# Performance work log

Measured on AMD Instinct MI355X. Metric: run time of the kernel, lower is better.

The kernel has to match this reference:

```python
import jax, jax.numpy as jnp
import numpy as np

WINDOW = 7
EPS = 1e-8


def setup_inputs() -> dict:
    key = jax.random.key(0)
    k1, k2, k3 = jax.random.split(key, 3)
    x = jax.random.normal(k1, (8, 256, 64, 64), dtype=jnp.float32)
    # 1x1 conv weights (bias=False): [out_ch, in_ch]
    w_reduce = jax.random.normal(k2, (64, 256), dtype=jnp.float32) * 0.05
    w_proj = jax.random.normal(k3, (512, 64), dtype=jnp.float32) * 0.1
    return {"x": x, "w_reduce": w_reduce, "w_proj": w_proj}


def _unfold_window(feat, window):
    # feat: [b, c, h, w] -> patches: [b, c, window*window, h, w]
    b, c, h, w = feat.shape
    pad = window // 2
    fp = jnp.pad(feat, ((0, 0), (0, 0), (pad, pad), (pad, pad)))
    # fixed small loop over window^2 = 49 shifts (matches F.unfold ordering)
    return jnp.stack(
        [fp[:, :, i:i + h, j:j + w] for i in range(window) for j in range(window)],
        axis=2,
    )


def reference(x, w_reduce, w_proj):
    window = WINDOW
    # reduce: 1x1 conv, no bias
    feat = jnp.einsum('oc,bchw->bohw', w_reduce, x)  # [b, cr, h, w]
    patches = _unfold_window(feat, window)           # [b, cr, K, h, w], K=49
    # cosine similarity between center feature and each window patch (dim=channel)
    dot = jnp.einsum('bchw,bckhw->bkhw', feat, patches)          # [b, K, h, w]
    cn = jnp.sqrt(jnp.sum(feat * feat, axis=1))                  # [b, h, w]
    pn = jnp.sqrt(jnp.sum(patches * patches, axis=1))            # [b, K, h, w]
    sim = dot / jnp.maximum(cn[:, None] * pn, EPS)               # [b, K, h, w]
    att = jax.nn.softmax(sim, axis=1)                            # softmax over window dim
    corr = jnp.einsum('bkhw,bckhw->bchw', att, patches)          # [b, cr, h, w]
    # proj: 1x1 conv, no bias
    return jnp.einsum('oc,bchw->bohw', w_proj, corr)             # [b, out, h, w]
```

## Files before the change

### kernel.cpp

```cpp
#include <hip/hip_runtime.h>
#include <stdint.h>

#define NPIX 4096
#define CIN  256
#define CR   64
#define COUT 512
#define NB   8
#define CG   256
#define FT   128

typedef _Float16 half8 __attribute__((ext_vector_type(8)));
typedef _Float16 half4 __attribute__((ext_vector_type(4)));
typedef _Float16 half2v __attribute__((ext_vector_type(2)));
typedef float f32x4 __attribute__((ext_vector_type(4)));

__device__ __forceinline__ float dpp8_sum(float d) {
  int y;
  y = __builtin_amdgcn_update_dpp(0, __float_as_int(d), 0xB1, 0xF, 0xF, true);
  d += __int_as_float(y);
  y = __builtin_amdgcn_update_dpp(0, __float_as_int(d), 0x4E, 0xF, 0xF, true);
  d += __int_as_float(y);
  y = __builtin_amdgcn_update_dpp(0, __float_as_int(d), 0x141, 0xF, 0xF, true);
  d += __int_as_float(y);
  return d;
}

__global__ __launch_bounds__(256) void k0_prep(
    const float* __restrict__ wr, const float* __restrict__ wp,
    _Float16* __restrict__ wrAh, _Float16* __restrict__ wrAl,
    _Float16* __restrict__ wpH,
    float* __restrict__ icnG, float* __restrict__ featTail)
{
  const int tid = blockIdx.x * 256 + threadIdx.x;
  if (tid < 16384) {
    const int j = tid & 7, l = (tid >> 3) & 63;
    const int kt = (tid >> 9) & 7, mt = tid >> 12;
    const int m = mt * 16 + (l & 15);
    const int k = kt * 32 + (l >> 4) * 8 + j;
    const float v = wr[m * CIN + k];
    const _Float16 h = (_Float16)v;
    wrAh[tid] = h;
    wrAl[tid] = (_Float16)(v - (float)h);
  } else if (tid < 16384 + COUT * CR) {
    const int fi = tid - 16384;
    const int j = fi & 7, l = (fi >> 3) & 63;
    const int kt = (fi >> 9) & 1, ot = (fi >> 10) & 3, g = fi >> 12;
    const int o = g * 64 + ot * 16 + (l & 15);
    const int k = kt * 32 + (l >> 4) * 8 + j;
    wpH[fi] = (_Float16)wp[o * CR + k];
  } else {
    const int gi = tid - (16384 + COUT * CR);
    if (gi < CG)               icnG[gi] = 0.f;
    else if (gi < 2 * CG)      icnG[CG + NB * NPIX + (gi - CG)] = 0.f;
    else if (gi < 2 * CG + FT) featTail[gi - 2 * CG] = 0.f;
  }
}

__global__ __launch_bounds__(512) void k1_reduce(
    const float* __restrict__ x,
    const _Float16* __restrict__ wrAh, const _Float16* __restrict__ wrAl,
    _Float16* __restrict__ feat_h, float* __restrict__ icn)
{
  const int blk = blockIdx.x;
  const int b = blk >> 6, seg = blk & 63;
  const int t = threadIdx.x, lane = t & 63;
  const int g = __builtin_amdgcn_readfirstlane((int)t >> 6);
  const int nt = g & 3, mth = g >> 2;
  const int col = lane & 15, krow = lane >> 4;

  const float* xb = x + (size_t)b * CIN * NPIX + seg * 64 + nt * 16 + col;

  f32x4 c0 = {0.f, 0.f, 0.f, 0.f};
  f32x4 c1 = {0.f, 0.f, 0.f, 0.f};

#pragma unroll
  for (int kt = 0; kt < 8; ++kt) {
    half8 Bh, Bl;
    const float* xk = xb + (size_t)(kt * 32 + krow * 8) * NPIX;
#pragma unroll
    for (int j = 0; j < 8; ++j) {
      const float v = xk[(size_t)j * NPIX];
      const _Float16 h = (_Float16)v;
      Bh[j] = h;
      Bl[j] = (_Float16)(v - (float)h);
    }
    const int fi0 = ((mth * 2 + 0) * 8 + kt) * 512 + lane * 8;
    const int fi1 = ((mth * 2 + 1) * 8 + kt) * 512 + lane * 8;
    const half8 Ah0 = *(const half8*)(wrAh + fi0);
    const half8 Al0 = *(const half8*)(wrAl + fi0);
    const half8 Ah1 = *(const half8*)(wrAh + fi1);
    const half8 Al1 = *(const half8*)(wrAl + fi1);
    c0 = __builtin_amdgcn_mfma_f32_16x16x32_f16(Ah0, Bh, c0, 0, 0, 0);
    c0 = __builtin_amdgcn_mfma_f32_16x16x32_f16(Ah0, Bl, c0, 0, 0, 0);
    c0 = __builtin_amdgcn_mfma_f32_16x16x32_f16(Al0, Bh, c0, 0, 0, 0);
    c1 = __builtin_amdgcn_mfma_f32_16x16x32_f16(Ah1, Bh, c1, 0, 0, 0);
    c1 = __builtin_amdgcn_mfma_f32_16x16x32_f16(Ah1, Bl, c1, 0, 0, 0);
    c1 = __builtin_amdgcn_mfma_f32_16x16x32_f16(Al1, Bh, c1, 0, 0, 0);
  }

  const int px = seg * 64 + nt * 16 + col;
  _Float16* fb = feat_h + ((size_t)b * NPIX + px) * 64;
  const int ch0 = mth * 32 + krow * 4;
  half4 v0, v1;
  float p = 0.f;
#pragma unroll
  for (int r = 0; r < 4; ++r) {
    v0[r] = (_Float16)c0[r];
    v1[r] = (_Float16)c1[r];
    p = fmaf(c0[r], c0[r], p);
    p = fmaf(c1[r], c1[r], p);
  }
  *(half4*)(fb + ch0) = v0;
  *(half4*)(fb + ch0 + 16) = v1;

  p += __shfl_xor(p, 16);
  p += __shfl_xor(p, 32);

  __shared__ float cn[8][16];
  if (lane < 16) cn[g][lane] = p;
  __syncthreads();
  if (t < 64) {
    const int nt2 = t >> 4, c16 = t & 15;
    const float ss = cn[nt2][c16] + cn[nt2 + 4][c16];
    icn[b * NPIX + seg * 64 + t] = rsqrtf(fmaxf(ss, 1e-16f));
  }
}

__global__ __launch_bounds__(256, 4) void k23_fused(
    const _Float16* __restrict__ feat_h, const float* __restrict__ icn,
    const _Float16* __restrict__ wpH, float* __restrict__ out)
{
  const int blk = blockIdx.x;
  const int b = blk & 7;
  const int rest = blk >> 3;
  const int h = rest >> 1, s = rest & 1;
  const int t = threadIdx.x;
  const int lane = t & 63;
  const int wv = __builtin_amdgcn_readfirstlane((int)t >> 6);
  const int w = t >> 3;
  const int cb = (t & 7) * 8;
  const int wg = s * 32 + w;
  const int px = h * 64 + wg;
  const int gpx = b * NPIX + px;

  const float* cnb = icn + b * NPIX;

  __shared__ __align__(16) _Float16 fs[2][40][72];
  __shared__ float cnS[2][48];
  __shared__ __align__(16) _Float16 corrH[2048];

  half8 rS0, rS1;
  float ricn = 0.f;

  auto LOAD = [&](int ar) {
    const long base = ((long)b * NPIX + ar * 64 + s * 32 - 4) * 64;
    rS0 = *(const half8*)(feat_h + base + (long)t * 8);
    if (t < 64) rS1 = *(const half8*)(feat_h + base + (long)(256 + t) * 8);
    if (t < 40) ricn = cnb[ar * 64 + s * 32 - 4 + t];
  };
  auto WRITE = [&](int bufi) {
    *(half8*)&fs[bufi][t >> 3][(t & 7) * 8] = rS0;
    if (t < 64) *(half8*)&fs[bufi][32 + (t >> 3)][(t & 7) * 8] = rS1;
    if (t < 40) cnS[bufi][t] = ricn;
  };

  half2v fc2[4];
  {
    const half8 fcv = *(const half8*)(feat_h + ((size_t)b * NPIX + px) * 64 + cb);
#pragma unroll
    for (int i = 0; i < 4; ++i) { fc2[i][0] = fcv[2*i]; fc2[i][1] = fcv[2*i+1]; }
  }
  const float icnc = icn[gpx];

  half2v accA[4], accB[4];
#pragma unroll
  for (int i = 0; i < 4; ++i) {
    accA[i] = (half2v)(_Float16)0.f;
    accB[i] = (half2v)(_Float16)0.f;
  }

  const int lo = (h - 3 < 0) ? 0 : h - 3;
  const int hi = (h + 3 > 63) ? 63 : h + 3;
  float l = 7.0f * (float)(6 - (hi - lo));

  LOAD(lo);
  WRITE(0);
  __syncthreads();

  int buf = 0;
  for (int ar = lo; ar <= hi; ++ar) {
    if (ar < hi) LOAD(ar + 1);
#pragma unroll
    for (int dx = -3; dx <= 3; ++dx) {
      const int j = w + 4 + dx;
      const half8 nv = *(const half8*)&fs[buf][j][cb];
      half2v n0, n1, n2, n3;
      n0[0] = nv[0]; n0[1] = nv[1];
      n1[0] = nv[2]; n1[1] = nv[3];
      n2[0] = nv[4]; n2[1] = nv[5];
      n3[0] = nv[6]; n3[1] = nv[7];
      float d = 0.f;
      d = __builtin_amdgcn_fdot2(fc2[0], n0, d, false);
      d = __builtin_amdgcn_fdot2(fc2[1], n1, d, false);
      d = __builtin_amdgcn_fdot2(fc2[2], n2, d, false);
      d = __builtin_amdgcn_fdot2(fc2[3], n3, d, false);
      d = dpp8_sum(d);
      const float icnk = cnS[buf][j];
      float sim = d * icnc * icnk;
      const bool valid = (unsigned)(wg + dx) < 64u;
      sim = valid ? sim : 0.f;
      const float p = __expf(sim);
      l += p;
      const float pv = valid ? p : 0.f;
      const _Float16 ph = (_Float16)pv;
      half2v ph2; ph2[0] = ph; ph2[1] = ph;
      if (dx & 1) {
        accA[0] = ph2 * n0 + accA[0];
        accA[1] = ph2 * n1 + accA[1];
        accA[2] = ph2 * n2 + accA[2];
        accA[3] = ph2 * n3 + accA[3];
      } else {
        accB[0] = ph2 * n0 + accB[0];
        accB[1] = ph2 * n1 + accB[1];
        accB[2] = ph2 * n2 + accB[2];
        accB[3] = ph2 * n3 + accB[3];
      }
    }
    if (ar < hi) WRITE(buf ^ 1);
    __syncthreads();
    buf ^= 1;
  }

  {
    const float inv = __builtin_amdgcn_rcpf(l);
    half8 hv;
#pragma unroll
    for (int i = 0; i < 4; ++i) {
      const float a0 = (float)accA[i][0] + (float)accB[i][0];
      const float a1 = (float)accA[i][1] + (float)accB[i][1];
      hv[2*i]   = (_Float16)(a0 * inv);
      hv[2*i+1] = (_Float16)(a1 * inv);
    }
    const int wbyte = (w * 128 + (cb << 1)) ^ ((w & 7) << 4);
    *(half8*)((char*)corrH + wbyte) = hv;
  }
  __syncthreads();

  const char* cH = (const char*)corrH;
#pragma unroll
  for (int pt = 0; pt < 2; ++pt) {
    half8 Bf0, Bf1;
    {
      const int pxl = pt * 16 + (lane & 15);
      const int sw = (pxl & 7) << 4;
      const int rowb = pxl * 128 + ((lane >> 4) << 4);
      Bf0 = *(const half8*)(cH + (rowb ^ sw));
      Bf1 = *(const half8*)(cH + ((rowb + 64) ^ sw));
    }
#pragma unroll
    for (int ot = 0; ot < 8; ++ot) {
      const int T = wv * 8 + ot;
      f32x4 c = {0.f, 0.f, 0.f, 0.f};
      const half8 A0 = *(const half8*)(wpH + (size_t)(T * 2 + 0) * 512 + lane * 8);
      const half8 A1 = *(const half8*)(wpH + (size_t)(T * 2 + 1) * 512 + lane * 8);
      c = __builtin_amdgcn_mfma_f32_16x16x32_f16(A0, Bf0, c, 0, 0, 0);
      c = __builtin_amdgcn_mfma_f32_16x16x32_f16(A1, Bf1, c, 0, 0, 0);
      float* op = out + ((size_t)b * COUT + T * 16 + ((lane >> 4) << 2)) * NPIX
                      + h * 64 + s * 32 + pt * 16 + (lane & 15);
#pragma unroll
      for (int r = 0; r < 4; ++r) op[(size_t)r * NPIX] = c[r];
    }
  }
}

extern "C" void kernel_launch(void* const* d_in, const int* in_sizes, int n_in,
                              void* d_out, int out_size, void* d_ws, size_t ws_size,
                              hipStream_t stream)
{
  const float* x  = (const float*)d_in[0];
  const float* wr = (const float*)d_in[1];
  const float* wp = (const float*)d_in[2];
  float* out = (float*)d_out;

  float* ws = (float*)d_ws;
  _Float16* wrAh  = (_Float16*)ws;
  _Float16* wrAl  = (_Float16*)(ws + 8192);
  _Float16* wpH   = (_Float16*)(ws + 16384);
  float* icnG     = ws + 32768;
  float* icn      = icnG + CG;
  _Float16* feat_h = (_Float16*)(icn + NB * NPIX + CG);
  float* featTail = (float*)(feat_h + (size_t)NB * NPIX * 64);

  hipLaunchKernelGGL(k0_prep,   dim3(195),  dim3(256), 0, stream, wr, wp, wrAh, wrAl, wpH, icnG, featTail);
  hipLaunchKernelGGL(k1_reduce, dim3(512),  dim3(512), 0, stream, x, wrAh, wrAl, feat_h, icn);
  hipLaunchKernelGGL(k23_fused, dim3(1024), dim3(256), 0, stream, feat_h, icn, wpH, out);
}
```

Before: 39.79 us.

## Prefetch two rows ahead and reuse weight fragments across pixel tiles

The row-staging pipeline now keeps two rows of global loads in flight in registers (distance-2 prefetch), so global latency is hidden over a longer compute span. The projection loop is restructured so each weight fragment pair is loaded once and applied to both 16-pixel tiles, halving global weight loads, with s_setprio raised around the MFMA block. Stores from both tiles are interleaved. This costs extra registers for the second prefetch buffer, which could reduce occupancy.

```diff
diff --git a/kernel.cpp b/kernel.cpp
--- a/kernel.cpp
+++ b/kernel.cpp
@@ -149,19 +149,25 @@
   __shared__ float cnS[2][48];
   __shared__ __align__(16) _Float16 corrH[2048];
 
-  half8 rS0, rS1;
-  float ricn = 0.f;
-
-  auto LOAD = [&](int ar) {
+  half8 pS0, pS1, nS0, nS1;
+  float pIc = 0.f, nIc = 0.f;
+
+  auto LOADP = [&](int ar) {
     const long base = ((long)b * NPIX + ar * 64 + s * 32 - 4) * 64;
-    rS0 = *(const half8*)(feat_h + base + (long)t * 8);
-    if (t < 64) rS1 = *(const half8*)(feat_h + base + (long)(256 + t) * 8);
-    if (t < 40) ricn = cnb[ar * 64 + s * 32 - 4 + t];
+    pS0 = *(const half8*)(feat_h + base + (long)t * 8);
+    if (t < 64) pS1 = *(const half8*)(feat_h + base + (long)(256 + t) * 8);
+    if (t < 40) pIc = cnb[ar * 64 + s * 32 - 4 + t];
   };
-  auto WRITE = [&](int bufi) {
-    *(half8*)&fs[bufi][t >> 3][(t & 7) * 8] = rS0;
-    if (t < 64) *(half8*)&fs[bufi][32 + (t >> 3)][(t & 7) * 8] = rS1;
-    if (t < 40) cnS[bufi][t] = ricn;
+  auto LOADN = [&](int ar) {
+    const long base = ((long)b * NPIX + ar * 64 + s * 32 - 4) * 64;
+    nS0 = *(const half8*)(feat_h + base + (long)t * 8);
+    if (t < 64) nS1 = *(const half8*)(feat_h + base + (long)(256 + t) * 8);
+    if (t < 40) nIc = cnb[ar * 64 + s * 32 - 4 + t];
+  };
+  auto WRITEP = [&](int bufi) {
+    *(half8*)&fs[bufi][t >> 3][(t & 7) * 8] = pS0;
+    if (t < 64) *(half8*)&fs[bufi][32 + (t >> 3)][(t & 7) * 8] = pS1;
+    if (t < 40) cnS[bufi][t] = pIc;
   };
 
   half2v fc2[4];
@@ -183,13 +189,14 @@
   const int hi = (h + 3 > 63) ? 63 : h + 3;
   float l = 7.0f * (float)(6 - (hi - lo));
 
-  LOAD(lo);
-  WRITE(0);
+  LOADP(lo);
+  WRITEP(0);
+  LOADP(lo + 1);
   __syncthreads();
 
   int buf = 0;
   for (int ar = lo; ar <= hi; ++ar) {
-    if (ar < hi) LOAD(ar + 1);
+    if (ar + 2 <= hi) LOADN(ar + 2);
 #pragma unroll
     for (int dx = -3; dx <= 3; ++dx) {
       const int j = w + 4 + dx;
@@ -226,9 +233,10 @@
         accB[3] = ph2 * n3 + accB[3];
       }
     }
-    if (ar < hi) WRITE(buf ^ 1);
+    if (ar + 1 <= hi) WRITEP(buf ^ 1);
     __syncthreads();
     buf ^= 1;
+    pS0 = nS0; pS1 = nS1; pIc = nIc;
   }
 
   {
@@ -247,28 +255,38 @@
   __syncthreads();
 
   const char* cH = (const char*)corrH;
-#pragma unroll
-  for (int pt = 0; pt < 2; ++pt) {
-    half8 Bf0, Bf1;
-    {
-      const int pxl = pt * 16 + (lane & 15);
-      const int sw = (pxl & 7) << 4;
-      const int rowb = pxl * 128 + ((lane >> 4) << 4);
-      Bf0 = *(const half8*)(cH + (rowb ^ sw));
-      Bf1 = *(const half8*)(cH + ((rowb + 64) ^ sw));
-    }
-#pragma unroll
-    for (int ot = 0; ot < 8; ++ot) {
-      const int T = wv * 8 + ot;
-      f32x4 c = {0.f, 0.f, 0.f, 0.f};
-      const half8 A0 = *(const half8*)(wpH + (size_t)(T * 2 + 0) * 512 + lane * 8);
-      const half8 A1 = *(const half8*)(wpH + (size_t)(T * 2 + 1) * 512 + lane * 8);
-      c = __builtin_amdgcn_mfma_f32_16x16x32_f16(A0, Bf0, c, 0, 0, 0);
-      c = __builtin_amdgcn_mfma_f32_16x16x32_f16(A1, Bf1, c, 0, 0, 0);
-      float* op = out + ((size_t)b * COUT + T * 16 + ((lane >> 4) << 2)) * NPIX
-                      + h * 64 + s * 32 + pt * 16 + (lane & 15);
-#pragma unroll
-      for (int r = 0; r < 4; ++r) op[(size_t)r * NPIX] = c[r];
+  half8 Bf00, Bf01, Bf10, Bf11;
+  {
+    const int pxl0 = (lane & 15);
+    const int sw0 = (pxl0 & 7) << 4;
+    const int rowb0 = pxl0 * 128 + ((lane >> 4) << 4);
+    Bf00 = *(const half8*)(cH + (rowb0 ^ sw0));
+    Bf01 = *(const half8*)(cH + ((rowb0 + 64) ^ sw0));
+    const int pxl1 = 16 + (lane & 15);
+    const int sw1 = (pxl1 & 7) << 4;
+    const int rowb1 = pxl1 * 128 + ((lane >> 4) << 4);
+    Bf10 = *(const half8*)(cH + (rowb1 ^ sw1));
+    Bf11 = *(const half8*)(cH + ((rowb1 + 64) ^ sw1));
+  }
+#pragma unroll
+  for (int ot = 0; ot < 8; ++ot) {
+    const int T = wv * 8 + ot;
+    const half8 A0 = *(const half8*)(wpH + (size_t)(T * 2 + 0) * 512 + lane * 8);
+    const half8 A1 = *(const half8*)(wpH + (size_t)(T * 2 + 1) * 512 + lane * 8);
+    f32x4 c0 = {0.f, 0.f, 0.f, 0.f};
+    f32x4 c1 = {0.f, 0.f, 0.f, 0.f};
+    __builtin_amdgcn_s_setprio(1);
+    c0 = __builtin_amdgcn_mfma_f32_16x16x32_f16(A0, Bf00, c0, 0, 0, 0);
+    c0 = __builtin_amdgcn_mfma_f32_16x16x32_f16(A1, Bf01, c0, 0, 0, 0);
+    c1 = __builtin_amdgcn_mfma_f32_16x16x32_f16(A0, Bf10, c1, 0, 0, 0);
+    c1 = __builtin_amdgcn_mfma_f32_16x16x32_f16(A1, Bf11, c1, 0, 0, 0);
+    __builtin_amdgcn_s_setprio(0);
+    float* op0 = out + ((size_t)b * COUT + T * 16 + ((lane >> 4) << 2)) * NPIX
+                     + h * 64 + s * 32 + (lane & 15);
+#pragma unroll
+    for (int r = 0; r < 4; ++r) {
+      op0[(size_t)r * NPIX] = c0[r];
+      op0[(size_t)r * NPIX + 16] = c1[r];
     }
   }
 }
```

After: 37.97 us. -4.6%, faster.
